# Kernel optimization log

Hardware: AMD Instinct MI355X
Metric: run time of the kernel (lower is better)

The kernel has to match this reference:

```python
import jax, jax.numpy as jnp
import numpy as np

N_IMG, M_GT, P_PROP = 16, 128, 8192
NUM_CLASSES = 80
THRESH_LO, THRESH_HI = 0.3, 0.7  # cfg.MODEL.ROI_HEADS.IOU_THRESHOLDS


def _make_boxes(key, shape, coord_scale=1000.0, wh_scale=200.0):
    k1, k2 = jax.random.split(key)
    xy = jax.random.uniform(k1, shape[:-1] + (2,)) * coord_scale
    wh = jax.random.uniform(k2, shape[:-1] + (2,)) * wh_scale + 1.0
    return jnp.concatenate([xy, xy + wh], axis=-1)  # [..., 4] = x1,y1,x2,y2


def setup_inputs() -> dict:
    key = jax.random.key(0)
    kg, kp, kc, ki = jax.random.split(key, 4)
    gt_boxes = _make_boxes(kg, (N_IMG, M_GT, 4))
    proposal_boxes = _make_boxes(kp, (N_IMG, P_PROP, 4))
    gt_classes = jax.random.randint(kc, (N_IMG, M_GT), 0, NUM_CLASSES, dtype=jnp.int32)
    gt_ignores = jax.random.randint(ki, (N_IMG, M_GT), 0, 2) > 0  # bool
    return {
        "gt_boxes": gt_boxes,
        "proposal_boxes": proposal_boxes,
        "gt_classes": gt_classes,
        "gt_ignores": gt_ignores,
    }


def _pairwise_iou(gt, pr):
    # gt: [N, M, 4], pr: [N, P, 4] -> iou [N, M, P]
    area_g = (gt[..., 2] - gt[..., 0]) * (gt[..., 3] - gt[..., 1])  # [N, M]
    area_p = (pr[..., 2] - pr[..., 0]) * (pr[..., 3] - pr[..., 1])  # [N, P]
    lt = jnp.maximum(gt[:, :, None, :2], pr[:, None, :, :2])  # [N, M, P, 2]
    rb = jnp.minimum(gt[:, :, None, 2:], pr[:, None, :, 2:])
    wh = jnp.clip(rb - lt, 0.0)
    inter = wh[..., 0] * wh[..., 1]  # [N, M, P]
    union = area_g[:, :, None] + area_p[:, None, :] - inter
    return jnp.where(inter > 0, inter / jnp.maximum(union, 1e-9), 0.0)


def reference(gt_boxes, proposal_boxes, gt_classes, gt_ignores):
    iou = _pairwise_iou(gt_boxes, proposal_boxes)  # [N, M, P]

    # Matcher: best GT per proposal + threshold labels (0=bg, -1=ignore, 1=fg)
    matched_vals = jnp.max(iou, axis=1)               # [N, P]
    matched_idxs = jnp.argmax(iou, axis=1).astype(jnp.int32)  # [N, P]
    matched_labels = jnp.where(
        matched_vals >= THRESH_HI, 1,
        jnp.where(matched_vals >= THRESH_LO, -1, 0),
    ).astype(jnp.int32)

    # gt_ignores toggling: proposals overlapping an ignored GT above high thresh -> -1
    neg_inf = jnp.float32(-1e30)
    max_ig = jnp.max(jnp.where(gt_ignores[:, :, None], iou, neg_inf), axis=1)  # [N, P]
    matched_labels = jnp.where(max_ig > THRESH_HI, -1, matched_labels)

    # _sample_proposals label assignment (full vector; random subsampling omitted)
    prop_gt_classes = jnp.take_along_axis(gt_classes, matched_idxs, axis=1)  # [N, P]
    prop_gt_classes = jnp.where(matched_labels == 0, NUM_CLASSES, prop_gt_classes)
    prop_gt_classes = jnp.where(matched_labels == -1, -1, prop_gt_classes)

    return iou, matched_idxs, matched_labels, prop_gt_classes
```

## Files before the change

### kernel.cpp

```cpp
#include <hip/hip_runtime.h>

#define N_IMG 16
#define M_GT 128
#define P_PROP 8192
#define NUM_CLASSES 80
#define THREADS 256

__global__ __launch_bounds__(THREADS) void roi_match_kernel(
    const float* __restrict__ gt_boxes,
    const float* __restrict__ pr_boxes,
    const int*   __restrict__ gt_classes,
    const void*  __restrict__ gt_ignores,
    float* __restrict__ out)
{
    __shared__ float s_x1[M_GT], s_y1[M_GT], s_x2[M_GT], s_y2[M_GT], s_ag[M_GT];
    __shared__ int   s_cls[M_GT], s_ign[M_GT];
    __shared__ int   s_b01, s_bf;

    const int tid = threadIdx.x;
    const int n   = blockIdx.x >> 5;
    const int p   = ((blockIdx.x & 31) << 8) + tid;

    if (tid == 0) { s_b01 = 0; s_bf = 0; }
    __syncthreads();
    {
        const int* w = (const int*)gt_ignores;
        int bad01 = 0, badf = 0;
        for (int i = tid; i < 512; i += THREADS) {
            int v = w[i];
            bad01 |= (v != 0) & (v != 1);
            badf  |= (v != 0) & (v != 0x3F800000);
        }
        if (bad01) atomicOr(&s_b01, 1);
        if (badf)  atomicOr(&s_bf, 1);
    }
    __syncthreads();
    const int mode = s_b01 ? (s_bf ? 1 : 2) : 0;

    for (int m = tid; m < M_GT; m += THREADS) {
        const float4 g = *reinterpret_cast<const float4*>(gt_boxes + ((size_t)n * M_GT + m) * 4);
        s_x1[m] = g.x; s_y1[m] = g.y; s_x2[m] = g.z; s_y2[m] = g.w;
        s_ag[m] = (g.z - g.x) * (g.w - g.y);
        s_cls[m] = gt_classes[n * M_GT + m];
        int ig;
        if (mode == 0)      ig = ((const int*)gt_ignores)[n * M_GT + m] != 0;
        else if (mode == 1) ig = ((const unsigned char*)gt_ignores)[n * M_GT + m] != 0;
        else                ig = ((const float*)gt_ignores)[n * M_GT + m] != 0.0f;
        s_ign[m] = ig;
    }
    __syncthreads();

    const float4 pv = *reinterpret_cast<const float4*>(pr_boxes + ((size_t)n * P_PROP + p) * 4);
    const float px1 = pv.x, py1 = pv.y, px2 = pv.z, py2 = pv.w;
    const float area_p = (px2 - px1) * (py2 - py1);

    float best  = -1.0f;
    int   bidx  = 0;
    float maxig = -1e30f;

    float* iou_out = out + (size_t)(n * M_GT) * P_PROP + p;

#pragma unroll 8
    for (int m = 0; m < M_GT; ++m) {
        const float lx = fmaxf(s_x1[m], px1);
        const float ly = fmaxf(s_y1[m], py1);
        const float rx = fminf(s_x2[m], px2);
        const float ry = fminf(s_y2[m], py2);
        const float w  = fmaxf(rx - lx, 0.0f);
        const float h  = fmaxf(ry - ly, 0.0f);
        const float inter = w * h;
        const float uni   = s_ag[m] + area_p - inter;
        const float iou   = (inter > 0.0f) ? inter / fmaxf(uni, 1e-9f) : 0.0f;

        iou_out[(size_t)m * P_PROP] = iou;

        if (iou > best) { best = iou; bidx = m; }
        if (s_ign[m]) maxig = fmaxf(maxig, iou);
    }

    int label = (best >= 0.7f) ? 1 : ((best >= 0.3f) ? -1 : 0);
    if (maxig > 0.7f) label = -1;

    int cls = s_cls[bidx];
    if (label == 0)  cls = NUM_CLASSES;
    if (label == -1) cls = -1;

    const size_t base = (size_t)N_IMG * M_GT * P_PROP;
    const int np = n * P_PROP + p;
    out[base + np]                      = (float)bidx;
    out[base + (size_t)N_IMG * P_PROP + np]     = (float)label;
    out[base + (size_t)2 * N_IMG * P_PROP + np] = (float)cls;
}

extern "C" void kernel_launch(void* const* d_in, const int* in_sizes, int n_in,
                              void* d_out, int out_size, void* d_ws, size_t ws_size,
                              hipStream_t stream) {
    const float* gt_boxes   = (const float*)d_in[0];
    const float* pr_boxes   = (const float*)d_in[1];
    const int*   gt_classes = (const int*)d_in[2];
    const void*  gt_ignores = (const void*)d_in[3];
    float* out = (float*)d_out;

    const int blocks = N_IMG * (P_PROP / THREADS);
    roi_match_kernel<<<blocks, THREADS, 0, stream>>>(
        gt_boxes, pr_boxes, gt_classes, gt_ignores, out);
}
```

Measured before the change: 100.8 us.

## Split GT dimension across blocks with separate reduction kernel

```diff
diff --git a/kernel.cpp b/kernel.cpp
--- a/kernel.cpp
+++ b/kernel.cpp
@@ -6,20 +6,29 @@
 #define NUM_CLASSES 80
 #define THREADS 256
 
-__global__ __launch_bounds__(THREADS) void roi_match_kernel(
+#define QUARTERS 4
+#define MQ (M_GT / QUARTERS)
+#define PPT 2
+#define PBLK (THREADS * PPT)
+#define NPBLK (P_PROP / PBLK)
+#define NP (N_IMG * P_PROP)
+
+__global__ __launch_bounds__(THREADS) void iou_kernel(
     const float* __restrict__ gt_boxes,
     const float* __restrict__ pr_boxes,
-    const int*   __restrict__ gt_classes,
     const void*  __restrict__ gt_ignores,
-    float* __restrict__ out)
+    float* __restrict__ out,
+    float* __restrict__ ws)
 {
-    __shared__ float s_x1[M_GT], s_y1[M_GT], s_x2[M_GT], s_y2[M_GT], s_ag[M_GT];
-    __shared__ int   s_cls[M_GT], s_ign[M_GT];
-    __shared__ int   s_b01, s_bf;
+    __shared__ float4 s_box[MQ];
+    __shared__ float  s_ag[MQ];
+    __shared__ int    s_ign[MQ];
+    __shared__ int    s_b01, s_bf;
 
-    const int tid = threadIdx.x;
-    const int n   = blockIdx.x >> 5;
-    const int p   = ((blockIdx.x & 31) << 8) + tid;
+    const int tid  = threadIdx.x;
+    const int q    = blockIdx.x & 3;
+    const int pblk = (blockIdx.x >> 2) & (NPBLK - 1);
+    const int n    = blockIdx.x >> 6;
 
     if (tid == 0) { s_b01 = 0; s_bf = 0; }
     __syncthreads();
@@ -37,59 +46,102 @@
     __syncthreads();
     const int mode = s_b01 ? (s_bf ? 1 : 2) : 0;
 
-    for (int m = tid; m < M_GT; m += THREADS) {
+    if (tid < MQ) {
+        const int m = q * MQ + tid;
         const float4 g = *reinterpret_cast<const float4*>(gt_boxes + ((size_t)n * M_GT + m) * 4);
-        s_x1[m] = g.x; s_y1[m] = g.y; s_x2[m] = g.z; s_y2[m] = g.w;
-        s_ag[m] = (g.z - g.x) * (g.w - g.y);
-        s_cls[m] = gt_classes[n * M_GT + m];
+        s_box[tid] = g;
+        s_ag[tid]  = (g.z - g.x) * (g.w - g.y);
         int ig;
         if (mode == 0)      ig = ((const int*)gt_ignores)[n * M_GT + m] != 0;
         else if (mode == 1) ig = ((const unsigned char*)gt_ignores)[n * M_GT + m] != 0;
         else                ig = ((const float*)gt_ignores)[n * M_GT + m] != 0.0f;
-        s_ign[m] = ig;
+        s_ign[tid] = ig;
     }
     __syncthreads();
 
-    const float4 pv = *reinterpret_cast<const float4*>(pr_boxes + ((size_t)n * P_PROP + p) * 4);
-    const float px1 = pv.x, py1 = pv.y, px2 = pv.z, py2 = pv.w;
-    const float area_p = (px2 - px1) * (py2 - py1);
+    const int p0 = pblk * PBLK + tid * PPT;
+    const float4 pa = *reinterpret_cast<const float4*>(pr_boxes + ((size_t)n * P_PROP + p0) * 4);
+    const float4 pb = *reinterpret_cast<const float4*>(pr_boxes + ((size_t)n * P_PROP + p0 + 1) * 4);
+    const float area_a = (pa.z - pa.x) * (pa.w - pa.y);
+    const float area_b = (pb.z - pb.x) * (pb.w - pb.y);
 
-    float best  = -1.0f;
-    int   bidx  = 0;
-    float maxig = -1e30f;
+    float best_a = -1.0f, best_b = -1.0f;
+    int   arg_a  = 0,     arg_b  = 0;
+    float ig_a   = -1e30f, ig_b  = -1e30f;
 
-    float* iou_out = out + (size_t)(n * M_GT) * P_PROP + p;
+    float* iou_out = out + ((size_t)(n * M_GT + q * MQ)) * P_PROP + p0;
 
 #pragma unroll 8
-    for (int m = 0; m < M_GT; ++m) {
-        const float lx = fmaxf(s_x1[m], px1);
-        const float ly = fmaxf(s_y1[m], py1);
-        const float rx = fminf(s_x2[m], px2);
-        const float ry = fminf(s_y2[m], py2);
-        const float w  = fmaxf(rx - lx, 0.0f);
-        const float h  = fmaxf(ry - ly, 0.0f);
-        const float inter = w * h;
-        const float uni   = s_ag[m] + area_p - inter;
-        const float iou   = (inter > 0.0f) ? inter / fmaxf(uni, 1e-9f) : 0.0f;
+    for (int mi = 0; mi < MQ; ++mi) {
+        const float4 g  = s_box[mi];
+        const float  ag = s_ag[mi];
+        const int    ig = s_ign[mi];
+        const int    m  = q * MQ + mi;
 
-        iou_out[(size_t)m * P_PROP] = iou;
+        float lx = fmaxf(g.x, pa.x), ly = fmaxf(g.y, pa.y);
+        float rx = fminf(g.z, pa.z), ry = fminf(g.w, pa.w);
+        float w  = fmaxf(rx - lx, 0.0f), h = fmaxf(ry - ly, 0.0f);
+        float inter = w * h;
+        float uni   = ag + area_a - inter;
+        float iou_a = (inter > 0.0f) ? inter / fmaxf(uni, 1e-9f) : 0.0f;
 
-        if (iou > best) { best = iou; bidx = m; }
-        if (s_ign[m]) maxig = fmaxf(maxig, iou);
+        lx = fmaxf(g.x, pb.x); ly = fmaxf(g.y, pb.y);
+        rx = fminf(g.z, pb.z); ry = fminf(g.w, pb.w);
+        w  = fmaxf(rx - lx, 0.0f); h = fmaxf(ry - ly, 0.0f);
+        inter = w * h;
+        uni   = ag + area_b - inter;
+        float iou_b = (inter > 0.0f) ? inter / fmaxf(uni, 1e-9f) : 0.0f;
+
+        *reinterpret_cast<float2*>(iou_out) = make_float2(iou_a, iou_b);
+        iou_out += P_PROP;
+
+        if (iou_a > best_a) { best_a = iou_a; arg_a = m; }
+        if (iou_b > best_b) { best_b = iou_b; arg_b = m; }
+        if (ig) { ig_a = fmaxf(ig_a, iou_a); ig_b = fmaxf(ig_b, iou_b); }
+    }
+
+    const size_t idx = (size_t)q * NP + (size_t)n * P_PROP + p0;
+    float* wval = ws;
+    float* warg = ws + (size_t)QUARTERS * NP;
+    float* wig  = ws + (size_t)2 * QUARTERS * NP;
+    *reinterpret_cast<float2*>(wval + idx) = make_float2(best_a, best_b);
+    *reinterpret_cast<float2*>(warg + idx) = make_float2((float)arg_a, (float)arg_b);
+    *reinterpret_cast<float2*>(wig  + idx) = make_float2(ig_a, ig_b);
+}
+
+__global__ __launch_bounds__(THREADS) void reduce_kernel(
+    const float* __restrict__ ws,
+    const int*   __restrict__ gt_classes,
+    float* __restrict__ out)
+{
+    const int t = blockIdx.x * THREADS + threadIdx.x;
+    const int n = t >> 13;
+
+    const float* wval = ws;
+    const float* warg = ws + (size_t)QUARTERS * NP;
+    const float* wig  = ws + (size_t)2 * QUARTERS * NP;
+
+    float best = -1.0f, barg = 0.0f, mig = -1e30f;
+#pragma unroll
+    for (int q = 0; q < QUARTERS; ++q) {
+        const float v = wval[(size_t)q * NP + t];
+        const float a = warg[(size_t)q * NP + t];
+        const float g = wig [(size_t)q * NP + t];
+        if (v > best) { best = v; barg = a; }
+        mig = fmaxf(mig, g);
     }
 
     int label = (best >= 0.7f) ? 1 : ((best >= 0.3f) ? -1 : 0);
-    if (maxig > 0.7f) label = -1;
+    if (mig > 0.7f) label = -1;
 
-    int cls = s_cls[bidx];
+    int cls = gt_classes[n * M_GT + (int)barg];
     if (label == 0)  cls = NUM_CLASSES;
     if (label == -1) cls = -1;
 
     const size_t base = (size_t)N_IMG * M_GT * P_PROP;
-    const int np = n * P_PROP + p;
-    out[base + np]                      = (float)bidx;
-    out[base + (size_t)N_IMG * P_PROP + np]     = (float)label;
-    out[base + (size_t)2 * N_IMG * P_PROP + np] = (float)cls;
+    out[base + t]            = barg;
+    out[base + NP + t]       = (float)label;
+    out[base + 2 * (size_t)NP + t] = (float)cls;
 }
 
 extern "C" void kernel_launch(void* const* d_in, const int* in_sizes, int n_in,
@@ -100,8 +152,11 @@
     const int*   gt_classes = (const int*)d_in[2];
     const void*  gt_ignores = (const void*)d_in[3];
     float* out = (float*)d_out;
+    float* ws  = (float*)d_ws;
 
-    const int blocks = N_IMG * (P_PROP / THREADS);
-    roi_match_kernel<<<blocks, THREADS, 0, stream>>>(
-        gt_boxes, pr_boxes, gt_classes, gt_ignores, out);
+    const int blocks_main = N_IMG * NPBLK * QUARTERS;
+    iou_kernel<<<blocks_main, THREADS, 0, stream>>>(gt_boxes, pr_boxes, gt_ignores, out, ws);
+
+    const int blocks_red = NP / THREADS;
+    reduce_kernel<<<blocks_red, THREADS, 0, stream>>>(ws, gt_classes, out);
 }
```

Result: faster. 96.73 us (-4.0%).
